# Performance work log

Measured on AMD Instinct MI355X. Metric: run time of the kernel, lower is better.

The kernel has to match this reference:

```python
import jax, jax.numpy as jnp
import numpy as np

B, CIN, H, W = 8, 512, 32, 32
NH = 8
DQ = DK = DV = 256  # int(0.5 * Cin)
COUT = 512


def setup_inputs() -> dict:
    key = jax.random.key(0)
    k0, k1, k2, k3, k4 = jax.random.split(key, 5)
    x = jax.random.normal(k0, (B, CIN, H, W), dtype=jnp.float32)
    # 1x1 conv weights stored as [out, in] matrices (kernel size 1)
    w_qkv = jax.random.normal(k1, (DQ + DK + DV, CIN), dtype=jnp.float32) * 0.02
    b_qkv = jax.random.normal(k2, (DQ + DK + DV,), dtype=jnp.float32) * 0.02
    w_attn = jax.random.normal(k3, (COUT, DV), dtype=jnp.float32) * 0.02
    b_attn = jax.random.normal(k4, (COUT,), dtype=jnp.float32) * 0.02
    return {"x": x, "w_qkv": w_qkv, "b_qkv": b_qkv, "w_attn": w_attn, "b_attn": b_attn}


def _split_heads(t):
    b, c, h, w = t.shape
    return t.reshape(b, NH, c // NH, h, w)


def reference(x, w_qkv, b_qkv, w_attn, b_attn):
    b, _, h, w = x.shape
    hw = h * w
    # 1x1 conv == per-pixel GEMM
    qkv = jnp.einsum('bchw,oc->bohw', x, w_qkv) + b_qkv[None, :, None, None]
    q = qkv[:, :DQ]
    k = qkv[:, DQ:DQ + DK]
    v = qkv[:, DQ + DK:]
    dkh = DK // NH
    q = _split_heads(q) * (dkh ** -0.5)
    k = _split_heads(k)
    v = _split_heads(v)
    flat_q = q.reshape(b, NH, DQ // NH, hw)
    flat_k = k.reshape(b, NH, DK // NH, hw)
    flat_v = v.reshape(b, NH, DV // NH, hw)
    # logits: [b, NH, hw, hw]  (q^T k over feature dim)
    logits = jnp.einsum('bndq,bndk->bnqk', flat_q, flat_k)
    # FAITHFUL quirk: softmax over the HEAD axis (dim=1), as in the source
    weights = jax.nn.softmax(logits, axis=1)
    # attn_out: [b, NH, hw, dvh]
    attn_out = jnp.einsum('bnqk,bndk->bnqd', weights, flat_v)
    # FAITHFUL quirk: raw reshape (no transpose) to [b, NH, dvh, H, W]
    attn_out = attn_out.reshape(b, NH, DV // NH, h, w).reshape(b, DV, h, w)
    out = jnp.einsum('bchw,oc->bohw', attn_out, w_attn) + b_attn[None, :, None, None]
    return out
```

## Files before the change

### kernel.cpp

```cpp
#include <hip/hip_runtime.h>
#include <math.h>

#define BATCH 8
#define CIN   512
#define DQKV  768
#define NHEAD 8
#define HW    1024

typedef __attribute__((ext_vector_type(8))) short  short8;
typedef __attribute__((ext_vector_type(4))) float  float4v;

__device__ __forceinline__ ushort f2bf(float f) {
    union { float f; unsigned u; } c; c.f = f;
    unsigned u = c.u + 0x7fffu + ((c.u >> 16) & 1u);
    return (ushort)(u >> 16);
}

__device__ __forceinline__ void async_ld16(const ushort* g, ushort* l) {
    auto gp = (const __attribute__((address_space(1))) unsigned int*)g;
    auto lp = (__attribute__((address_space(3))) unsigned int*)l;
    __builtin_amdgcn_global_load_lds(gp, lp, 16, 0, 0);
}

__global__ __launch_bounds__(256)
void transpose_cvt(const float* __restrict__ in, ushort* __restrict__ out,
                   int K, int N)
{
    __shared__ float Ts[64][65];
    const int b  = blockIdx.z;
    const int k0 = blockIdx.y * 64;
    const int n0 = blockIdx.x * 64;
    const int t  = threadIdx.x;
    const float* ib = in + (size_t)b * K * N;
    ushort*      ob = out + (size_t)b * N * K;

    const int r  = t >> 4;
    const int c4 = (t & 15) * 4;
    #pragma unroll
    for (int p = 0; p < 4; ++p) {
        float4 v = *(const float4*)(ib + (size_t)(k0 + r + 16 * p) * N + n0 + c4);
        Ts[r + 16 * p][c4 + 0] = v.x;
        Ts[r + 16 * p][c4 + 1] = v.y;
        Ts[r + 16 * p][c4 + 2] = v.z;
        Ts[r + 16 * p][c4 + 3] = v.w;
    }
    __syncthreads();

    const int nl = t >> 3;
    const int kc = (t & 7) * 8;
    #pragma unroll
    for (int p = 0; p < 2; ++p) {
        int n = nl + 32 * p;
        uint4 u;
        u.x = (uint)f2bf(Ts[kc + 0][n]) | ((uint)f2bf(Ts[kc + 1][n]) << 16);
        u.y = (uint)f2bf(Ts[kc + 2][n]) | ((uint)f2bf(Ts[kc + 3][n]) << 16);
        u.z = (uint)f2bf(Ts[kc + 4][n]) | ((uint)f2bf(Ts[kc + 5][n]) << 16);
        u.w = (uint)f2bf(Ts[kc + 6][n]) | ((uint)f2bf(Ts[kc + 7][n]) << 16);
        *(uint4*)(ob + (size_t)(n0 + n) * K + k0 + kc) = u;
    }
}

__global__ void cvt_bf16(const float* __restrict__ in, ushort* __restrict__ out, int n8)
{
    int i = blockIdx.x * blockDim.x + threadIdx.x;
    if (i >= n8) return;
    const float4* p = (const float4*)(in + (size_t)i * 8);
    float4 a = p[0], b = p[1];
    uint4 u;
    u.x = (uint)f2bf(a.x) | ((uint)f2bf(a.y) << 16);
    u.y = (uint)f2bf(a.z) | ((uint)f2bf(a.w) << 16);
    u.z = (uint)f2bf(b.x) | ((uint)f2bf(b.y) << 16);
    u.w = (uint)f2bf(b.z) | ((uint)f2bf(b.w) << 16);
    *(uint4*)(out + (size_t)i * 8) = u;
}

__global__ __launch_bounds__(256)
void qk_transform(const ushort* __restrict__ qkv, ushort* __restrict__ Qt,
                  ushort* __restrict__ Kt)
{
    __shared__ ushort Ts[32 * 264];
    const int b   = blockIdx.z;
    const int g   = blockIdx.y;
    const int sp0 = blockIdx.x * 256;
    const int t   = threadIdx.x;

    const ushort* src = qkv + ((size_t)b * DQKV + g * 32) * HW;
    ushort* dst = (g < 8 ? Qt : Kt) + ((size_t)b * NHEAD + (g & 7)) * (HW * 32);

    #pragma unroll
    for (int p = 0; p < 4; ++p) {
        int d = (t >> 5) + p * 8;
        int c = t & 31;
        uint4 u = *(const uint4*)(src + (size_t)d * HW + sp0 + c * 8);
        *(uint4*)&Ts[d * 264 + c * 8] = u;
    }
    __syncthreads();

    ushort* orow = dst + (size_t)(sp0 + t) * 32;
    #pragma unroll
    for (int c = 0; c < 4; ++c) {
        ushort v[8];
        #pragma unroll
        for (int j = 0; j < 8; ++j) v[j] = Ts[(c * 8 + j) * 264 + t];
        *(uint4*)(orow + c * 8) = *(uint4*)v;
    }
}

template<int M, int K, bool QSCALE, bool OUTBF>
__global__ __launch_bounds__(256, 2)
void gemm_bt(const ushort* __restrict__ A, const ushort* __restrict__ Bt,
             const float* __restrict__ bias, void* __restrict__ Oo)
{
    __shared__ __align__(16) ushort As[128 * 64];
    __shared__ __align__(16) ushort Bs[128 * 64];

    const int b    = blockIdx.z;
    const int m0   = blockIdx.y * 128;
    const int n0   = blockIdx.x * 128;
    const int t    = threadIdx.x;
    const int lane = t & 63;
    const int wave = t >> 6;
    const int l16  = lane & 15;
    const int quad = lane >> 4;
    const int wm   = (wave & 1) * 64;
    const int wn   = (wave >> 1) * 64;

    const ushort* Bb = Bt + (size_t)b * HW * K;

    float4v acc[4][4];
    #pragma unroll
    for (int i = 0; i < 4; ++i)
        #pragma unroll
        for (int j = 0; j < 4; ++j)
            acc[i][j] = (float4v){0.f, 0.f, 0.f, 0.f};

    const int srow = t >> 3;
    const int sg   = t & 7;

    for (int k0 = 0; k0 < K; k0 += 64) {
        __syncthreads();
        #pragma unroll
        for (int is = 0; is < 4; ++is) {
            int row = srow + is * 32;
            int gch = sg ^ (row & 7);
            async_ld16(A  + (size_t)(m0 + row) * K + k0 + gch * 8,
                       As + (size_t)t * 8 + is * 2048);
            async_ld16(Bb + (size_t)(n0 + row) * K + k0 + gch * 8,
                       Bs + (size_t)t * 8 + is * 2048);
        }
        __syncthreads();

        #pragma unroll
        for (int ks = 0; ks < 2; ++ks) {
            short8 af[4], bf[4];
            #pragma unroll
            for (int i = 0; i < 4; ++i) {
                int row = wm + i * 16 + l16;
                int ch  = (ks * 4 + quad) ^ (row & 7);
                af[i] = *(const short8*)&As[row * 64 + ch * 8];
            }
            #pragma unroll
            for (int j = 0; j < 4; ++j) {
                int row = wn + j * 16 + l16;
                int ch  = (ks * 4 + quad) ^ (row & 7);
                bf[j] = *(const short8*)&Bs[row * 64 + ch * 8];
            }
            #pragma unroll
            for (int i = 0; i < 4; ++i)
                #pragma unroll
                for (int j = 0; j < 4; ++j)
                    acc[i][j] = __builtin_amdgcn_mfma_f32_16x16x32_bf16(
                        af[i], bf[j], acc[i][j], 0, 0, 0);
        }
    }

    #pragma unroll
    for (int i = 0; i < 4; ++i) {
        #pragma unroll
        for (int rr = 0; rr < 4; ++rr) {
            int m = m0 + wm + i * 16 + quad * 4 + rr;
            float bi = bias[m];
            float sc = QSCALE ? ((m < 256) ? 0.17677669529663687f : 1.0f) : 1.0f;
            #pragma unroll
            for (int j = 0; j < 4; ++j) {
                int n = n0 + wn + j * 16 + l16;
                float val = (acc[i][j][rr] + bi) * sc;
                if (OUTBF)
                    ((ushort*)Oo)[((size_t)b * M + m) * HW + n] = f2bf(val);
                else
                    ((float*)Oo)[((size_t)b * M + m) * HW + n] = val;
            }
        }
    }
}

#define WROW 136
#define OROW 132

__global__ __launch_bounds__(512, 4)
void attn_kernel(const ushort* __restrict__ qkv, const ushort* __restrict__ Qt,
                 const ushort* __restrict__ Kt, ushort* __restrict__ ab)
{
    __shared__ __align__(16) ushort Ws[NHEAD * 16 * WROW];

    const int t    = threadIdx.x;
    const int b    = blockIdx.y;
    const int j    = blockIdx.x >> 1;
    const int uh   = blockIdx.x & 1;
    const int wave = t >> 6;
    const int lane = t & 63;
    const int l16  = lane & 15;
    const int quad = lane >> 4;

    const ushort* Vb  = qkv + ((size_t)b * DQKV + 512) * HW;
    const ushort* Qtb = Qt + (size_t)b * (NHEAD * HW * 32);
    const ushort* Ktb = Kt + (size_t)b * (NHEAD * HW * 32);

    const int qlane = (uh * 16 + l16) * 32 + j;
    short8 qf[NHEAD];
    #pragma unroll
    for (int h = 0; h < NHEAD; ++h)
        qf[h] = *(const short8*)(Qtb + ((size_t)h * HW + qlane) * 32 + quad * 8);

    float4v oacc[2];
    oacc[0] = (float4v){0.f, 0.f, 0.f, 0.f};
    oacc[1] = (float4v){0.f, 0.f, 0.f, 0.f};

    for (int k0 = 0; k0 < HW; k0 += 128) {
        const int kk = k0 + wave * 16 + l16;
        float4v S[NHEAD];
        #pragma unroll
        for (int h = 0; h < NHEAD; ++h) {
            short8 kf = *(const short8*)(Ktb + ((size_t)h * HW + kk) * 32 + quad * 8);
            S[h] = __builtin_amdgcn_mfma_f32_16x16x32_bf16(
                kf, qf[h], (float4v){0.f, 0.f, 0.f, 0.f}, 0, 0, 0);
        }

        float4v mx = S[0];
        #pragma unroll
        for (int h = 1; h < NHEAD; ++h)
            #pragma unroll
            for (int r = 0; r < 4; ++r) mx[r] = fmaxf(mx[r], S[h][r]);
        float4v sum = (float4v){0.f, 0.f, 0.f, 0.f};
        #pragma unroll
        for (int h = 0; h < NHEAD; ++h)
            #pragma unroll
            for (int r = 0; r < 4; ++r) {
                S[h][r] = __expf(S[h][r] - mx[r]);
                sum[r] += S[h][r];
            }
        float4v inv;
        #pragma unroll
        for (int r = 0; r < 4; ++r) inv[r] = __builtin_amdgcn_rcpf(sum[r]);
        uint2 wpk[NHEAD];
        #pragma unroll
        for (int h = 0; h < NHEAD; ++h) {
            wpk[h].x = (uint)f2bf(S[h][0] * inv[0]) | ((uint)f2bf(S[h][1] * inv[1]) << 16);
            wpk[h].y = (uint)f2bf(S[h][2] * inv[2]) | ((uint)f2bf(S[h][3] * inv[3]) << 16);
        }

        __syncthreads();

        #pragma unroll
        for (int h = 0; h < NHEAD; ++h)
            *(uint2*)&Ws[(size_t)(h * 16 + l16) * WROW + wave * 16 + quad * 4] = wpk[h];

        __syncthreads();

        #pragma unroll
        for (int ks = 0; ks < 4; ++ks) {
            short8 wf = *(const short8*)&Ws[(size_t)(wave * 16 + l16) * WROW + ks * 32 + quad * 8];
            #pragma unroll
            for (int ds = 0; ds < 2; ++ds) {
                short8 vf = *(const short8*)(Vb + (size_t)(wave * 32 + ds * 16 + l16) * HW
                                             + k0 + ks * 32 + quad * 8);
                oacc[ds] = __builtin_amdgcn_mfma_f32_16x16x32_bf16(wf, vf, oacc[ds], 0, 0, 0);
            }
        }
    }

    __syncthreads();
    ushort* Ot = Ws;
    #pragma unroll
    for (int ds = 0; ds < 2; ++ds) {
        int d = ds * 16 + l16;
        #pragma unroll
        for (int r = 0; r < 4; ++r)
            Ot[(size_t)d * OROW + wave * 16 + quad * 4 + r] = f2bf(oacc[ds][r]);
    }
    __syncthreads();

    {
        int d  = t >> 4;
        int c8 = (t & 15) * 8;
        uint2 a = *(const uint2*)&Ot[(size_t)d * OROW + c8];
        uint2 b2 = *(const uint2*)&Ot[(size_t)d * OROW + c8 + 4];
        int h   = c8 >> 4;
        int col = h * 32 + uh * 16 + (c8 & 15);
        uint4 u = make_uint4(a.x, a.y, b2.x, b2.y);
        *(uint4*)(ab + ((size_t)b * HW + j * 32 + d) * 256 + col) = u;
    }
}

extern "C" void kernel_launch(void* const* d_in, const int* in_sizes, int n_in,
                              void* d_out, int out_size, void* d_ws, size_t ws_size,
                              hipStream_t stream)
{
    const float* x      = (const float*)d_in[0];
    const float* w_qkv  = (const float*)d_in[1];
    const float* b_qkv  = (const float*)d_in[2];
    const float* w_attn = (const float*)d_in[3];
    const float* b_attn = (const float*)d_in[4];
    float* out = (float*)d_out;

    ushort* qkv_b = (ushort*)d_ws;
    ushort* xb    = qkv_b + 6291456;
    ushort* Qt    = xb;
    ushort* Kt    = xb + 2097152;
    ushort* ab    = xb + 4194304;
    ushort* wb1   = ab + 2097152;
    ushort* wb2   = wb1 + 393216;

    cvt_bf16<<<192, 256, 0, stream>>>(w_qkv, wb1, 49152);
    cvt_bf16<<<64, 256, 0, stream>>>(w_attn, wb2, 16384);
    transpose_cvt<<<dim3(16, 8, BATCH), 256, 0, stream>>>(x, xb, CIN, HW);

    gemm_bt<DQKV, CIN, true, true>
        <<<dim3(8, 6, BATCH), 256, 0, stream>>>(wb1, xb, b_qkv, qkv_b);

    qk_transform<<<dim3(4, 16, BATCH), 256, 0, stream>>>(qkv_b, Qt, Kt);

    attn_kernel<<<dim3(64, BATCH), 512, 0, stream>>>(qkv_b, Qt, Kt, ab);

    gemm_bt<512, 256, false, false>
        <<<dim3(8, 4, BATCH), 256, 0, stream>>>(wb2, ab, b_attn, out);
}
```

Before: 164.1 us.

## Fuse Q/K transpose into QKV GEMM epilogue and software-pipeline attention softmax

```diff
diff --git a/kernel.cpp b/kernel.cpp
--- a/kernel.cpp
+++ b/kernel.cpp
@@ -1,4 +1,5 @@
 #include <hip/hip_runtime.h>
+#include <hip/hip_bf16.h>
 #include <math.h>
 
 #define BATCH 8
@@ -14,6 +15,12 @@
     union { float f; unsigned u; } c; c.f = f;
     unsigned u = c.u + 0x7fffu + ((c.u >> 16) & 1u);
     return (ushort)(u >> 16);
+}
+
+__device__ __forceinline__ uint pkbf(float a, float b) {
+    union { __hip_bfloat162 h; uint u; } c;
+    c.h = __float22bfloat162_rn(make_float2(a, b));
+    return c.u;
 }
 
 __device__ __forceinline__ void async_ld16(const ushort* g, ushort* l) {
@@ -52,10 +59,10 @@
     for (int p = 0; p < 2; ++p) {
         int n = nl + 32 * p;
         uint4 u;
-        u.x = (uint)f2bf(Ts[kc + 0][n]) | ((uint)f2bf(Ts[kc + 1][n]) << 16);
-        u.y = (uint)f2bf(Ts[kc + 2][n]) | ((uint)f2bf(Ts[kc + 3][n]) << 16);
-        u.z = (uint)f2bf(Ts[kc + 4][n]) | ((uint)f2bf(Ts[kc + 5][n]) << 16);
-        u.w = (uint)f2bf(Ts[kc + 6][n]) | ((uint)f2bf(Ts[kc + 7][n]) << 16);
+        u.x = pkbf(Ts[kc + 0][n], Ts[kc + 1][n]);
+        u.y = pkbf(Ts[kc + 2][n], Ts[kc + 3][n]);
+        u.z = pkbf(Ts[kc + 4][n], Ts[kc + 5][n]);
+        u.w = pkbf(Ts[kc + 6][n], Ts[kc + 7][n]);
         *(uint4*)(ob + (size_t)(n0 + n) * K + k0 + kc) = u;
     }
 }
@@ -67,52 +74,24 @@
     const float4* p = (const float4*)(in + (size_t)i * 8);
     float4 a = p[0], b = p[1];
     uint4 u;
-    u.x = (uint)f2bf(a.x) | ((uint)f2bf(a.y) << 16);
-    u.y = (uint)f2bf(a.z) | ((uint)f2bf(a.w) << 16);
-    u.z = (uint)f2bf(b.x) | ((uint)f2bf(b.y) << 16);
-    u.w = (uint)f2bf(b.z) | ((uint)f2bf(b.w) << 16);
+    u.x = pkbf(a.x, a.y);
+    u.y = pkbf(a.z, a.w);
+    u.z = pkbf(b.x, b.y);
+    u.w = pkbf(b.z, b.w);
     *(uint4*)(out + (size_t)i * 8) = u;
 }
 
-__global__ __launch_bounds__(256)
-void qk_transform(const ushort* __restrict__ qkv, ushort* __restrict__ Qt,
-                  ushort* __restrict__ Kt)
-{
-    __shared__ ushort Ts[32 * 264];
-    const int b   = blockIdx.z;
-    const int g   = blockIdx.y;
-    const int sp0 = blockIdx.x * 256;
-    const int t   = threadIdx.x;
-
-    const ushort* src = qkv + ((size_t)b * DQKV + g * 32) * HW;
-    ushort* dst = (g < 8 ? Qt : Kt) + ((size_t)b * NHEAD + (g & 7)) * (HW * 32);
-
-    #pragma unroll
-    for (int p = 0; p < 4; ++p) {
-        int d = (t >> 5) + p * 8;
-        int c = t & 31;
-        uint4 u = *(const uint4*)(src + (size_t)d * HW + sp0 + c * 8);
-        *(uint4*)&Ts[d * 264 + c * 8] = u;
-    }
-    __syncthreads();
-
-    ushort* orow = dst + (size_t)(sp0 + t) * 32;
-    #pragma unroll
-    for (int c = 0; c < 4; ++c) {
-        ushort v[8];
-        #pragma unroll
-        for (int j = 0; j < 8; ++j) v[j] = Ts[(c * 8 + j) * 264 + t];
-        *(uint4*)(orow + c * 8) = *(uint4*)v;
-    }
-}
-
-template<int M, int K, bool QSCALE, bool OUTBF>
+#define TEW 136
+
+template<int M, int K, bool QSCALE, int OUTMODE>
 __global__ __launch_bounds__(256, 2)
 void gemm_bt(const ushort* __restrict__ A, const ushort* __restrict__ Bt,
-             const float* __restrict__ bias, void* __restrict__ Oo)
-{
-    __shared__ __align__(16) ushort As[128 * 64];
-    __shared__ __align__(16) ushort Bs[128 * 64];
+             const float* __restrict__ bias, void* __restrict__ Oo,
+             ushort* __restrict__ qt, ushort* __restrict__ kt)
+{
+    __shared__ __align__(16) ushort SH[16384];
+    ushort* As = SH;
+    ushort* Bs = SH + 8192;
 
     const int b    = blockIdx.z;
     const int m0   = blockIdx.y * 128;
@@ -174,21 +153,59 @@
         }
     }
 
-    #pragma unroll
-    for (int i = 0; i < 4; ++i) {
-        #pragma unroll
-        for (int rr = 0; rr < 4; ++rr) {
-            int m = m0 + wm + i * 16 + quad * 4 + rr;
-            float bi = bias[m];
-            float sc = QSCALE ? ((m < 256) ? 0.17677669529663687f : 1.0f) : 1.0f;
-            #pragma unroll
-            for (int j = 0; j < 4; ++j) {
-                int n = n0 + wn + j * 16 + l16;
-                float val = (acc[i][j][rr] + bi) * sc;
-                if (OUTBF)
-                    ((ushort*)Oo)[((size_t)b * M + m) * HW + n] = f2bf(val);
-                else
-                    ((float*)Oo)[((size_t)b * M + m) * HW + n] = val;
+    if (OUTMODE == 2 && m0 < 512) {
+        ushort* dst = (m0 < 256) ? qt : kt;
+        const int headbase = (m0 & 255) >> 5;
+        const float sc = (QSCALE && m0 < 256) ? 0.17677669529663687f : 1.0f;
+        #pragma unroll
+        for (int hn = 0; hn < 2; ++hn) {
+            __syncthreads();
+            if ((wave >> 1) == hn) {
+                #pragma unroll
+                for (int i = 0; i < 4; ++i) {
+                    int m_l = wm + i * 16 + quad * 4;
+                    float bi[4];
+                    #pragma unroll
+                    for (int rr = 0; rr < 4; ++rr) bi[rr] = bias[m0 + m_l + rr];
+                    #pragma unroll
+                    for (int j = 0; j < 4; ++j) {
+                        int n_l = j * 16 + l16;
+                        uint2 pk;
+                        pk.x = pkbf((acc[i][j][0] + bi[0]) * sc,
+                                    (acc[i][j][1] + bi[1]) * sc);
+                        pk.y = pkbf((acc[i][j][2] + bi[2]) * sc,
+                                    (acc[i][j][3] + bi[3]) * sc);
+                        *(uint2*)&SH[n_l * TEW + m_l] = pk;
+                    }
+                }
+            }
+            __syncthreads();
+            #pragma unroll
+            for (int p = 0; p < 4; ++p) {
+                int idx = p * 256 + t;
+                int d8 = idx & 3, h_l = (idx >> 2) & 3, n_l = idx >> 4;
+                uint4 u = *(const uint4*)&SH[n_l * TEW + h_l * 32 + d8 * 8];
+                size_t a = ((size_t)(b * NHEAD + headbase + h_l) * HW
+                            + (n0 + hn * 64 + n_l)) * 32 + d8 * 8;
+                *(uint4*)(dst + a) = u;
+            }
+        }
+    } else {
+        #pragma unroll
+        for (int i = 0; i < 4; ++i) {
+            #pragma unroll
+            for (int rr = 0; rr < 4; ++rr) {
+                int m = m0 + wm + i * 16 + quad * 4 + rr;
+                float bi = bias[m];
+                #pragma unroll
+                for (int j = 0; j < 4; ++j) {
+                    int n = n0 + wn + j * 16 + l16;
+                    float val = acc[i][j][rr] + bi;
+                    if (OUTMODE == 2)
+                        ((ushort*)Oo)[((size_t)b * 256 + (m & 255)) * HW + n] = f2bf(val);
+                    else
+                        ((float*)Oo)[((size_t)b * M + m) * HW + n] = val;
+                }
             }
         }
     }
@@ -198,7 +215,7 @@
 #define OROW 132
 
 __global__ __launch_bounds__(512, 4)
-void attn_kernel(const ushort* __restrict__ qkv, const ushort* __restrict__ Qt,
+void attn_kernel(const ushort* __restrict__ vb, const ushort* __restrict__ Qt,
                  const ushort* __restrict__ Kt, ushort* __restrict__ ab)
 {
     __shared__ __align__(16) ushort Ws[NHEAD * 16 * WROW];
@@ -212,7 +229,7 @@
     const int l16  = lane & 15;
     const int quad = lane >> 4;
 
-    const ushort* Vb  = qkv + ((size_t)b * DQKV + 512) * HW;
+    const ushort* Vb  = vb + (size_t)b * 256 * HW;
     const ushort* Qtb = Qt + (size_t)b * (NHEAD * HW * 32);
     const ushort* Ktb = Kt + (size_t)b * (NHEAD * HW * 32);
 
@@ -222,11 +239,7 @@
     for (int h = 0; h < NHEAD; ++h)
         qf[h] = *(const short8*)(Qtb + ((size_t)h * HW + qlane) * 32 + quad * 8);
 
-    float4v oacc[2];
-    oacc[0] = (float4v){0.f, 0.f, 0.f, 0.f};
-    oacc[1] = (float4v){0.f, 0.f, 0.f, 0.f};
-
-    for (int k0 = 0; k0 < HW; k0 += 128) {
+    auto compute_wpk = [&](int k0, uint2* wpk) {
         const int kk = k0 + wave * 16 + l16;
         float4v S[NHEAD];
         #pragma unroll
@@ -235,7 +248,6 @@
             S[h] = __builtin_amdgcn_mfma_f32_16x16x32_bf16(
                 kf, qf[h], (float4v){0.f, 0.f, 0.f, 0.f}, 0, 0, 0);
         }
-
         float4v mx = S[0];
         #pragma unroll
         for (int h = 1; h < NHEAD; ++h)
@@ -252,20 +264,31 @@
         float4v inv;
         #pragma unroll
         for (int r = 0; r < 4; ++r) inv[r] = __builtin_amdgcn_rcpf(sum[r]);
-        uint2 wpk[NHEAD];
         #pragma unroll
         for (int h = 0; h < NHEAD; ++h) {
-            wpk[h].x = (uint)f2bf(S[h][0] * inv[0]) | ((uint)f2bf(S[h][1] * inv[1]) << 16);
-            wpk[h].y = (uint)f2bf(S[h][2] * inv[2]) | ((uint)f2bf(S[h][3] * inv[3]) << 16);
-        }
-
-        __syncthreads();
-
+            wpk[h].x = pkbf(S[h][0] * inv[0], S[h][1] * inv[1]);
+            wpk[h].y = pkbf(S[h][2] * inv[2], S[h][3] * inv[3]);
+        }
+    };
+
+    float4v oacc[2];
+    oacc[0] = (float4v){0.f, 0.f, 0.f, 0.f};
+    oacc[1] = (float4v){0.f, 0.f, 0.f, 0.f};
+
+    {
+        uint2 w0[NHEAD];
+        compute_wpk(0, w0);
         #pragma unroll
         for (int h = 0; h < NHEAD; ++h)
-            *(uint2*)&Ws[(size_t)(h * 16 + l16) * WROW + wave * 16 + quad * 4] = wpk[h];
-
-        __syncthreads();
+            *(uint2*)&Ws[(size_t)(h * 16 + l16) * WROW + wave * 16 + quad * 4] = w0[h];
+    }
+    __syncthreads();
+
+    for (int i = 0; i < 8; ++i) {
+        const int k0 = i * 128;
+
+        uint2 nxt[NHEAD];
+        if (i < 7) compute_wpk(k0 + 128, nxt);
 
         #pragma unroll
         for (int ks = 0; ks < 4; ++ks) {
@@ -276,6 +299,14 @@
                                              + k0 + ks * 32 + quad * 8);
                 oacc[ds] = __builtin_amdgcn_mfma_f32_16x16x32_bf16(wf, vf, oacc[ds], 0, 0, 0);
             }
+        }
+
+        if (i < 7) {
+            __syncthreads();
+            #pragma unroll
+            for (int h = 0; h < NHEAD; ++h)
+                *(uint2*)&Ws[(size_t)(h * 16 + l16) * WROW + wave * 16 + quad * 4] = nxt[h];
+            __syncthreads();
         }
     }
 
@@ -313,25 +344,23 @@
     const float* b_attn = (const float*)d_in[4];
     float* out = (float*)d_out;
 
-    ushort* qkv_b = (ushort*)d_ws;
-    ushort* xb    = qkv_b + 6291456;
-    ushort* Qt    = xb;
-    ushort* Kt    = xb + 2097152;
-    ushort* ab    = xb + 4194304;
-    ushort* wb1   = ab + 2097152;
-    ushort* wb2   = wb1 + 393216;
+    ushort* vb  = (ushort*)d_ws;
+    ushort* xb  = vb + 2097152;
+    ushort* Qt  = xb + 4194304;
+    ushort* Kt  = Qt + 2097152;
+    ushort* ab  = Kt + 2097152;
+    ushort* wb1 = ab + 2097152;
+    ushort* wb2 = wb1 + 393216;
 
     cvt_bf16<<<192, 256, 0, stream>>>(w_qkv, wb1, 49152);
     cvt_bf16<<<64, 256, 0, stream>>>(w_attn, wb2, 16384);
     transpose_cvt<<<dim3(16, 8, BATCH), 256, 0, stream>>>(x, xb, CIN, HW);
 
-    gemm_bt<DQKV, CIN, true, true>
-        <<<dim3(8, 6, BATCH), 256, 0, stream>>>(wb1, xb, b_qkv, qkv_b);
-
-    qk_transform<<<dim3(4, 16, BATCH), 256, 0, stream>>>(qkv_b, Qt, Kt);
-
-    attn_kernel<<<dim3(64, BATCH), 512, 0, stream>>>(qkv_b, Qt, Kt, ab);
-
-    gemm_bt<512, 256, false, false>
-        <<<dim3(8, 4, BATCH), 256, 0, stream>>>(wb2, ab, b_attn, out);
-}
+    gemm_bt<DQKV, CIN, true, 2>
+        <<<dim3(8, 6, BATCH), 256, 0, stream>>>(wb1, xb, b_qkv, vb, Qt, Kt);
+
+    attn_kernel<<<dim3(64, BATCH), 512, 0, stream>>>(vb, Qt, Kt, ab);
+
+    gemm_bt<512, 256, false, 0>
+        <<<dim3(8, 4, BATCH), 256, 0, stream>>>(wb2, ab, b_attn, out, nullptr, nullptr);
+}
```

Measured after the change: 156.7 us. 1.05x faster.
